# Optimization experiments

Measured on AMD Instinct MI355X. Metric: run time of the kernel, lower is better.

The kernel has to match this reference:

```python
import jax, jax.numpy as jnp
import numpy as np

H = 2048      # hidden_size
NH = 32       # num attention heads
KVH = 8       # num kv heads
HD = 64       # head_dim
G = NH // KVH # kv groups (4)
EPS = 1e-6
THETA = 1000000.0


def _rms_norm(x, g):
    # normalize over last dim (head_dim)
    var = jnp.mean(jnp.square(x), axis=-1, keepdims=True)
    return x * jax.lax.rsqrt(var + EPS) * g


def _rope(seq_len, dtype):
    inv_freq = 1.0 / (THETA ** (jnp.arange(0, HD, 2, dtype=jnp.float32) / HD))
    pos = jnp.arange(seq_len, dtype=jnp.float32)
    freqs = pos[:, None] * inv_freq[None, :]          # [S, HD/2]
    emb = jnp.concatenate([freqs, freqs], axis=-1)    # [S, HD]
    return jnp.cos(emb).astype(dtype), jnp.sin(emb).astype(dtype)


def _rotate_half(x):
    x1, x2 = jnp.split(x, 2, axis=-1)
    return jnp.concatenate([-x2, x1], axis=-1)


def setup_inputs() -> dict:
    key = jax.random.key(0)
    ks = jax.random.split(key, 8)
    B, S = 1, 2048
    s = lambda fan_in: 1.0 / np.sqrt(fan_in)
    return {
        "hidden_states": jax.random.normal(ks[0], (B, S, H), jnp.float32),
        "Wq": jax.random.normal(ks[1], (H, NH * HD + NH), jnp.float32) * s(H),
        "Wk": jax.random.normal(ks[2], (H, KVH * HD), jnp.float32) * s(H),
        "Wv": jax.random.normal(ks[3], (H, KVH * HD), jnp.float32) * s(H),
        "Wo": jax.random.normal(ks[4], (NH * HD, H), jnp.float32) * s(NH * HD),
        "g_q": jnp.ones((HD,), jnp.float32),
        "g_k": jnp.ones((HD,), jnp.float32),
    }


def reference(hidden_states, Wq, Wk, Wv, Wo, g_q, g_k):
    B, S, _ = hidden_states.shape
    dtype = hidden_states.dtype

    qg = hidden_states @ Wq                              # [B,S,NH*HD+NH]
    k = hidden_states @ Wk                               # [B,S,KVH*HD]
    v = hidden_states @ Wv

    # headwise gate split, grouped per kv head (matches torch view/split)
    qg = qg.reshape(B, S, KVH, G * HD + G)
    q, gate = qg[..., : G * HD], qg[..., G * HD :]       # gate: [B,S,KVH,G]
    gate = gate.reshape(B, S, NH, 1)
    q = q.reshape(B, S, NH, HD).transpose(0, 2, 1, 3)    # [B,NH,S,HD]
    k = k.reshape(B, S, KVH, HD).transpose(0, 2, 1, 3)   # [B,KVH,S,HD]
    v = v.reshape(B, S, KVH, HD).transpose(0, 2, 1, 3)

    q = _rms_norm(q, g_q)
    k = _rms_norm(k, g_k)

    cos, sin = _rope(S, dtype)                           # [S,HD]
    cos, sin = cos[None, None], sin[None, None]
    q = q * cos + _rotate_half(q) * sin
    k = k * cos + _rotate_half(k) * sin

    # GQA: repeat kv heads
    k = jnp.repeat(k, G, axis=1)                         # [B,NH,S,HD]
    v = jnp.repeat(v, G, axis=1)

    # causal SDPA
    scale = 1.0 / np.sqrt(HD)
    scores = jnp.einsum("bhqd,bhkd->bhqk", q, k) * scale
    causal = jnp.tril(jnp.ones((S, S), bool))
    scores = jnp.where(causal[None, None], scores, jnp.finfo(dtype).min)
    probs = jax.nn.softmax(scores, axis=-1)
    attn = jnp.einsum("bhqk,bhkd->bhqd", probs, v)       # [B,NH,S,HD]

    attn = attn.transpose(0, 2, 1, 3)                    # [B,S,NH,HD]
    attn = attn * jax.nn.sigmoid(gate)
    attn = attn.reshape(B, S, NH * HD)
    return attn @ Wo
```

## Files before the change

### kernel.cpp

```cpp
#include <hip/hip_runtime.h>
#include <hip/hip_bf16.h>

#define SLEN 2048
#define HDIM 2048
#define NHEAD 32
#define KVHEAD 8
#define HEADD 64
#define NTOT 3104
#define NPAD 3200

typedef short bh8 __attribute__((ext_vector_type(8)));
typedef float f32x4 __attribute__((ext_vector_type(4)));

#define QSCALE 0.1803368801111204f

__device__ __forceinline__ unsigned short f2bf(float f) {
    union { float f; unsigned int u; } v; v.f = f;
    unsigned int u = v.u;
    return (unsigned short)((u + 0x7fffu + ((u >> 16) & 1u)) >> 16);
}

__device__ __forceinline__ unsigned int cvtpk_bf16(float lo, float hi) {
    unsigned int r;
    asm("v_cvt_pk_bf16_f32 %0, %1, %2" : "=v"(r) : "v"(lo), "v"(hi));
    return r;
}

__device__ __forceinline__ void gl_lds16(const unsigned short* g, unsigned short* l) {
    __builtin_amdgcn_global_load_lds(
        (const __attribute__((address_space(1))) unsigned int*)g,
        (__attribute__((address_space(3))) unsigned int*)l, 16, 0, 0);
}

__global__ void rope_tab_k(float* __restrict__ tab) {
    int i = blockIdx.x * 256 + threadIdx.x;
    int s = i >> 5, d = i & 31;
    float invf = __expf(-(float)d * (0.03125f * 13.815510557964274f));
    float ang = (float)s * invf;
    tab[(size_t)i * 2] = cosf(ang);
    tab[(size_t)i * 2 + 1] = sinf(ang);
}

__global__ void cast_x_k(const float* __restrict__ src, unsigned short* __restrict__ dst, int n) {
    int i = blockIdx.x * blockDim.x + threadIdx.x;
    int base = i * 4;
    if (base < n) {
        float4 f = *(const float4*)(src + base);
        ushort4 o;
        o.x = f2bf(f.x); o.y = f2bf(f.y); o.z = f2bf(f.z); o.w = f2bf(f.w);
        *(ushort4*)(dst + base) = o;
    }
}

__global__ void pack_wt_k(const float* __restrict__ Wq, const float* __restrict__ Wk,
                          const float* __restrict__ Wv, unsigned short* __restrict__ Wt) {
    __shared__ float tile[32][33];
    int n0 = blockIdx.x * 32, k0 = blockIdx.y * 32;
    int t = threadIdx.x;
    for (int i = 0; i < 4; i++) {
        int idx = i * 256 + t;
        int kr = idx >> 5, nc = idx & 31;
        int n = n0 + nc, k = k0 + kr;
        float val = 0.f;
        if (n < 2048)       { int h = n >> 6, d = n & 63; val = Wq[(size_t)k * 2080 + (h >> 2) * 260 + (h & 3) * 64 + d]; }
        else if (n < 2560)  { val = Wk[(size_t)k * 512 + (n - 2048)]; }
        else if (n < 3072)  { val = Wv[(size_t)k * 512 + (n - 2560)]; }
        else if (n < 3104)  { int h = n - 3072;           val = Wq[(size_t)k * 2080 + (h >> 2) * 260 + 256 + (h & 3)]; }
        tile[kr][nc] = val;
    }
    __syncthreads();
    for (int i = 0; i < 4; i++) {
        int idx = i * 256 + t;
        int nr = idx >> 5, kc = idx & 31;
        Wt[(size_t)(n0 + nr) * HDIM + (k0 + kc)] = f2bf(tile[kc][nr]);
    }
}

__global__ void pack_wot_k(const float* __restrict__ Wo, unsigned short* __restrict__ Wt) {
    __shared__ float tile[32][33];
    int n0 = blockIdx.x * 32, k0 = blockIdx.y * 32;
    int t = threadIdx.x;
    for (int i = 0; i < 4; i++) {
        int idx = i * 256 + t;
        int kr = idx >> 5, nc = idx & 31;
        tile[kr][nc] = Wo[(size_t)(k0 + kr) * 2048 + (n0 + nc)];
    }
    __syncthreads();
    for (int i = 0; i < 4; i++) {
        int idx = i * 256 + t;
        int nr = idx >> 5, kc = idx & 31;
        Wt[(size_t)(n0 + nr) * 2048 + (k0 + kc)] = f2bf(tile[kc][nr]);
    }
}

template<int NST, bool FUSE>
__global__ __launch_bounds__(256) void gemm_nt64_k(const unsigned short* __restrict__ A,
                                                   const unsigned short* __restrict__ Bt,
                                                   float* __restrict__ C0,
                                                   float* __restrict__ C1,
                                                   int ldc, int mtiles, int ntiles,
                                                   unsigned short* __restrict__ Qr,
                                                   unsigned short* __restrict__ Kr,
                                                   float* __restrict__ gate,
                                                   const float* __restrict__ g_q,
                                                   const float* __restrict__ g_k,
                                                   const float* __restrict__ tab) {
    const int K = 2048;
    __shared__ unsigned short As[3][64 * 32];
    __shared__ unsigned short Bs[3][128 * 32];
    int d = blockIdx.x;
    int nwg = gridDim.x;
    int cpx = nwg >> 3;
    int swz = (d & 7) * cpx + (d >> 3);
    int half = (swz >= ntiles) ? 1 : 0;
    int tile = swz - half * ntiles;
    int m0 = (tile % mtiles) * 64, n0 = (tile / mtiles) * 128;
    float* C = half ? C1 : C0;
    int koff = half * (NST * 32);
    int t = threadIdx.x;
    int w = t >> 6, l = t & 63;
    int wm = (w >> 1) * 32, wn = (w & 1) * 64;
    int lrow = l & 15, lc = l >> 4;
    int rsw = (lrow >> 1) & 3;
    int scol = ((l & 3) ^ ((l >> 3) & 3)) * 8;

    f32x4 acc[2][4];
    #pragma unroll
    for (int i = 0; i < 2; i++)
        #pragma unroll
        for (int j = 0; j < 4; j++)
            acc[i][j] = {0.f, 0.f, 0.f, 0.f};

    const unsigned short* ga = &A[(size_t)(m0 + w * 16 + (l >> 2)) * K + koff + scol];
    const unsigned short* gb = &Bt[(size_t)(n0 + w * 32 + (l >> 2)) * K + koff + scol];

#define STAGE_NT64(s, b) do { \
        gl_lds16(ga + (size_t)(s) * 32,                  &As[b][w * 512]); \
        gl_lds16(gb + (size_t)(s) * 32,                  &Bs[b][(w * 2 + 0) * 512]); \
        gl_lds16(gb + (size_t)(s) * 32 + 16 * (size_t)K, &Bs[b][(w * 2 + 1) * 512]); \
    } while (0)

#define GBODY(rb) do { \
        bh8 af[2], bb[4]; \
        _Pragma("unroll") \
        for (int i = 0; i < 2; i++) \
            af[i] = *(const bh8*)(&As[rb][(wm + i * 16 + lrow) * 32 + ((lc ^ rsw) * 8)]); \
        _Pragma("unroll") \
        for (int j = 0; j < 4; j++) \
            bb[j] = *(const bh8*)(&Bs[rb][(wn + j * 16 + lrow) * 32 + ((lc ^ rsw) * 8)]); \
        _Pragma("unroll") \
        for (int i = 0; i < 2; i++) \
            _Pragma("unroll") \
            for (int j = 0; j < 4; j++) \
                acc[i][j] = __builtin_amdgcn_mfma_f32_16x16x32_bf16(af[i], bb[j], acc[i][j], 0, 0, 0); \
    } while (0)

#define WB3 asm volatile("s_waitcnt vmcnt(3)\n\ts_barrier" ::: "memory")

    STAGE_NT64(0, 0);
    STAGE_NT64(1, 1);
    if constexpr (NST == 64) {
        for (int sb = 0; sb < 60; sb += 3) {
            WB3;
            STAGE_NT64(sb + 2, 2);
            GBODY(0);
            WB3;
            STAGE_NT64(sb + 3, 0);
            GBODY(1);
            WB3;
            STAGE_NT64(sb + 4, 1);
            GBODY(2);
        }
        WB3;
        STAGE_NT64(62, 2);
        GBODY(0);
        WB3;
        STAGE_NT64(63, 0);
        GBODY(1);
        WB3;
        GBODY(2);
        asm volatile("s_waitcnt vmcnt(0)\n\ts_barrier" ::: "memory");
        GBODY(0);
    } else {
        for (int sb = 0; sb < 30; sb += 3) {
            WB3;
            STAGE_NT64(sb + 2, 2);
            GBODY(0);
            WB3;
            STAGE_NT64(sb + 3, 0);
            GBODY(1);
            WB3;
            STAGE_NT64(sb + 4, 1);
            GBODY(2);
        }
        WB3;
        GBODY(0);
        asm volatile("s_waitcnt vmcnt(0)\n\ts_barrier" ::: "memory");
        GBODY(1);
    }
#undef WB3
#undef STAGE_NT64
#undef GBODY
    int col = l & 15, rbase = (l >> 4) * 4;
    if constexpr (FUSE) {
        int nt = n0 >> 7;
        if (nt < 20) {
            bool isQ = nt < 16;
            int hd = ((n0 + wn) - (isQ ? 0 : 2048)) >> 6;
            unsigned short* dst = (isQ ? Qr : Kr) + (size_t)hd * SLEN * 64;
            const float* gv = isQ ? g_q : g_k;
            float g0 = gv[col], g1 = gv[col + 16], g2 = gv[col + 32], g3 = gv[col + 48];
            float qs = isQ ? QSCALE : 1.0f;
            #pragma unroll
            for (int i = 0; i < 2; i++)
                #pragma unroll
                for (int r = 0; r < 4; r++) {
                    int s = m0 + wm + i * 16 + rbase + r;
                    float x0 = acc[i][0][r], x1 = acc[i][1][r];
                    float x2 = acc[i][2][r], x3 = acc[i][3][r];
                    float sq = x0 * x0 + x1 * x1 + x2 * x2 + x3 * x3;
                    sq += __shfl_xor(sq, 1);
                    sq += __shfl_xor(sq, 2);
                    sq += __shfl_xor(sq, 4);
                    sq += __shfl_xor(sq, 8);
                    float inv = rsqrtf(sq * (1.f / 64.f) + 1e-6f);
                    float xn0 = x0 * inv * g0, xn1 = x1 * inv * g1;
                    float xn2 = x2 * inv * g2, xn3 = x3 * inv * g3;
                    const float* te = tab + (size_t)s * 64;
                    float2 cs0 = *(const float2*)(te + col * 2);
                    float2 cs1 = *(const float2*)(te + (col + 16) * 2);
                    unsigned short* dr = dst + (size_t)s * 64;
                    dr[col]      = f2bf((xn0 * cs0.x - xn2 * cs0.y) * qs);
                    dr[col + 16] = f2bf((xn1 * cs1.x - xn3 * cs1.y) * qs);
                    dr[col + 32] = f2bf((xn2 * cs0.x + xn0 * cs0.y) * qs);
                    dr[col + 48] = f2bf((xn3 * cs1.x + xn1 * cs1.y) * qs);
                }
        } else if (nt < 24) {
            for (int i = 0; i < 2; i++)
                for (int j = 0; j < 4; j++)
                    #pragma unroll
                    for (int r = 0; r < 4; r++)
                        C[(size_t)(m0 + wm + i * 16 + rbase + r) * ldc + (n0 + wn + j * 16 + col)] = acc[i][j][r];
        } else {
            if (wn == 0) {
                #pragma unroll
                for (int i = 0; i < 2; i++)
                    #pragma unroll
                    for (int j = 0; j < 2; j++)
                        #pragma unroll
                        for (int r = 0; r < 4; r++) {
                            int s = m0 + wm + i * 16 + rbase + r;
                            int h = j * 16 + col;
                            gate[s * 32 + h] = 1.f / (1.f + __expf(-acc[i][j][r]));
                        }
            }
        }
    } else {
        for (int i = 0; i < 2; i++)
            for (int j = 0; j < 4; j++)
                #pragma unroll
                for (int r = 0; r < 4; r++)
                    C[(size_t)(m0 + wm + i * 16 + rbase + r) * ldc + (n0 + wn + j * 16 + col)] = acc[i][j][r];
    }
}

__global__ void addf4_k(const float* __restrict__ a, const float* __restrict__ b,
                        float* __restrict__ o) {
    int i = (blockIdx.x * 256 + threadIdx.x) * 4;
    float4 x = *(const float4*)(a + i);
    float4 y = *(const float4*)(b + i);
    float4 r; r.x = x.x + y.x; r.y = x.y + y.y; r.z = x.z + y.z; r.w = x.w + y.w;
    *(float4*)(o + i) = r;
}

__global__ void vt_k(const float* __restrict__ QKVG, unsigned short* __restrict__ Vt) {
    __shared__ float tile[64][65];
    int s0 = blockIdx.x * 64, hh = blockIdx.y;
    int t = threadIdx.x;
    #pragma unroll
    for (int i = 0; i < 4; i++) {
        int idx = i * 256 + t;
        int sr = idx >> 4, c4 = (idx & 15) * 4;
        float4 f = *(const float4*)(&QKVG[(size_t)(s0 + sr) * NPAD + 2560 + hh * 64 + c4]);
        tile[sr][c4] = f.x; tile[sr][c4 + 1] = f.y; tile[sr][c4 + 2] = f.z; tile[sr][c4 + 3] = f.w;
    }
    __syncthreads();
    #pragma unroll
    for (int i = 0; i < 4; i++) {
        int idx = i * 256 + t;
        int dr = idx >> 4, c4 = (idx & 15) * 4;
        int hb = c4 >> 5, f = (c4 >> 4) & 1, g = (c4 >> 2) & 3;
        int p = (hb * 4 + g) * 8 + f * 4;
        ushort4 o;
        o.x = f2bf(tile[c4][dr]); o.y = f2bf(tile[c4 + 1][dr]);
        o.z = f2bf(tile[c4 + 2][dr]); o.w = f2bf(tile[c4 + 3][dr]);
        *(ushort4*)(&Vt[((size_t)hh * 64 + dr) * SLEN + s0 + p]) = o;
    }
}

__global__ __launch_bounds__(256) void attn_k(const unsigned short* __restrict__ Qr,
                                              const unsigned short* __restrict__ Kr,
                                              const unsigned short* __restrict__ Vt,
                                              const float* __restrict__ gate,
                                              unsigned short* __restrict__ attn) {
    __shared__ unsigned short Kls[3][64 * 64];
    __shared__ unsigned short Vls[3][64 * 64];
    int d = blockIdx.x;
    int kvh = d & 7;
    int h = kvh * 4 + ((d >> 3) & 3);
    int qt = 31 - (d >> 5);
    int t = threadIdx.x, w = t >> 6, l = t & 63;
    int ql = l & 15, g = l >> 4;
    const float NEGINF = -__builtin_inff();

    const unsigned short* Kh = Kr + (size_t)kvh * SLEN * 64;
    const unsigned short* Vh = Vt + (size_t)kvh * 64 * SLEN;
    const unsigned short* Qh = Qr + (size_t)h * SLEN * 64;
    int lk = g * 8;
    int r8 = l >> 3, c8 = l & 7;
    int cs = 8 * (c8 ^ r8);
    int R0 = w * 16, R1 = w * 16 + 8;
    int rdswz = (ql & 7) << 4;

    int q0 = qt * 64;
    int qrow = q0 + w * 16 + ql;

    bh8 qa0 = *(const bh8*)(Qh + (size_t)qrow * 64 + lk);
    bh8 qa1 = *(const bh8*)(Qh + (size_t)qrow * 64 + 32 + lk);

    f32x4 o[4];
    #pragma unroll
    for (int i = 0; i < 4; i++) o[i] = {0.f, 0.f, 0.f, 0.f};
    float m2 = NEGINF, lsum = 0.f;

    int ntiles = qt + 1;
    {
        gl_lds16(&Kh[(size_t)(0 + R0 + r8) * 64 + cs], &Kls[0][R0 * 64]);
        gl_lds16(&Kh[(size_t)(0 + R1 + r8) * 64 + cs], &Kls[0][R1 * 64]);
        gl_lds16(&Vh[(size_t)(R0 + r8) * SLEN + 0 + cs], &Vls[0][R0 * 64]);
        gl_lds16(&Vh[(size_t)(R1 + r8) * SLEN + 0 + cs], &Vls[0][R1 * 64]);
    }
    if (ntiles > 1) {
        gl_lds16(&Kh[(size_t)(64 + R0 + r8) * 64 + cs], &Kls[1][R0 * 64]);
        gl_lds16(&Kh[(size_t)(64 + R1 + r8) * 64 + cs], &Kls[1][R1 * 64]);
        gl_lds16(&Vh[(size_t)(R0 + r8) * SLEN + 64 + cs], &Vls[1][R0 * 64]);
        gl_lds16(&Vh[(size_t)(R1 + r8) * SLEN + 64 + cs], &Vls[1][R1 * 64]);
    }
    int rd = 0, wr = 2;

    for (int ti = 0; ti < ntiles; ti++) {
        if (ti + 1 < ntiles) asm volatile("s_waitcnt vmcnt(4)\n\ts_barrier" ::: "memory");
        else                 asm volatile("s_waitcnt vmcnt(0)\n\ts_barrier" ::: "memory");
        if (ti + 2 < ntiles) {
            int kv1 = (ti + 2) * 64;
            gl_lds16(&Kh[(size_t)(kv1 + R0 + r8) * 64 + cs], &Kls[wr][R0 * 64]);
            gl_lds16(&Kh[(size_t)(kv1 + R1 + r8) * 64 + cs], &Kls[wr][R1 * 64]);
            gl_lds16(&Vh[(size_t)(R0 + r8) * SLEN + kv1 + cs], &Vls[wr][R0 * 64]);
            gl_lds16(&Vh[(size_t)(R1 + r8) * SLEN + kv1 + cs], &Vls[wr][R1 * 64]);
        }
        const unsigned short* Kb = &Kls[rd][0];
        const unsigned short* Vb = &Vls[rd][0];
        int kv0 = ti * 64;
        f32x4 sct[4];
        __builtin_amdgcn_s_setprio(1);
        #pragma unroll
        for (int nt = 0; nt < 4; nt++) {
            int rb = (nt * 16 + ql) * 128;
            bh8 kb0 = *(const bh8*)(&Kb[(rb + ((g * 16) ^ rdswz)) >> 1]);
            bh8 kb1 = *(const bh8*)(&Kb[(rb + ((64 + g * 16) ^ rdswz)) >> 1]);
            f32x4 a = {0.f, 0.f, 0.f, 0.f};
            a = __builtin_amdgcn_mfma_f32_16x16x32_bf16(kb0, qa0, a, 0, 0, 0);
            a = __builtin_amdgcn_mfma_f32_16x16x32_bf16(kb1, qa1, a, 0, 0, 0);
            sct[nt] = a;
        }
        __builtin_amdgcn_s_setprio(0);
        if (ti == qt) {
            #pragma unroll
            for (int nt = 0; nt < 4; nt++)
                #pragma unroll
                for (int j = 0; j < 4; j++) {
                    int key = kv0 + nt * 16 + 4 * g + j;
                    if (key > qrow) sct[nt][j] = NEGINF;
                }
        }
        float mt0 = fmaxf(fmaxf(sct[0][0], sct[0][1]), fmaxf(sct[0][2], sct[0][3]));
        float mt1 = fmaxf(fmaxf(sct[1][0], sct[1][1]), fmaxf(sct[1][2], sct[1][3]));
        float mt2 = fmaxf(fmaxf(sct[2][0], sct[2][1]), fmaxf(sct[2][2], sct[2][3]));
        float mt3 = fmaxf(fmaxf(sct[3][0], sct[3][1]), fmaxf(sct[3][2], sct[3][3]));
        float mt = fmaxf(fmaxf(mt0, mt1), fmaxf(mt2, mt3));
        mt = fmaxf(mt, __shfl_xor(mt, 16));
        mt = fmaxf(mt, __shfl_xor(mt, 32));
        if (!__all(mt - m2 <= 8.f)) {
            float mnew = fmaxf(m2, mt);
            float resc = __builtin_amdgcn_exp2f(m2 - mnew);
            m2 = mnew;
            lsum *= resc;
            float rf[4];
            #pragma unroll
            for (int j = 0; j < 4; j++) rf[j] = __shfl(resc, 4 * g + j);
            #pragma unroll
            for (int nt = 0; nt < 4; nt++) {
                f32x4 oo = o[nt];
                #pragma unroll
                for (int j = 0; j < 4; j++) oo[j] *= rf[j];
                o[nt] = oo;
            }
        }
        float ps = 0.f;
        #pragma unroll
        for (int nt = 0; nt < 4; nt++)
            #pragma unroll
            for (int j = 0; j < 4; j++) {
                float p = __builtin_amdgcn_exp2f(sct[nt][j] - m2);
                sct[nt][j] = p;
                ps += p;
            }
        ps += __shfl_xor(ps, 16);
        ps += __shfl_xor(ps, 32);
        lsum += ps;
        union { unsigned int u[4]; bh8 v; } pa0, pa1;
        pa0.u[0] = cvtpk_bf16(sct[0][0], sct[0][1]);
        pa0.u[1] = cvtpk_bf16(sct[0][2], sct[0][3]);
        pa0.u[2] = cvtpk_bf16(sct[1][0], sct[1][1]);
        pa0.u[3] = cvtpk_bf16(sct[1][2], sct[1][3]);
        pa1.u[0] = cvtpk_bf16(sct[2][0], sct[2][1]);
        pa1.u[1] = cvtpk_bf16(sct[2][2], sct[2][3]);
        pa1.u[2] = cvtpk_bf16(sct[3][0], sct[3][1]);
        pa1.u[3] = cvtpk_bf16(sct[3][2], sct[3][3]);
        __builtin_amdgcn_s_setprio(1);
        #pragma unroll
        for (int nt = 0; nt < 4; nt++) {
            int rb = (nt * 16 + ql) * 128;
            bh8 vb0 = *(const bh8*)(&Vb[(rb + ((g * 16) ^ rdswz)) >> 1]);
            bh8 vb1 = *(const bh8*)(&Vb[(rb + ((64 + g * 16) ^ rdswz)) >> 1]);
            o[nt] = __builtin_amdgcn_mfma_f32_16x16x32_bf16(pa0.v, vb0, o[nt], 0, 0, 0);
            o[nt] = __builtin_amdgcn_mfma_f32_16x16x32_bf16(pa1.v, vb1, o[nt], 0, 0, 0);
        }
        __builtin_amdgcn_s_setprio(0);
        rd = (rd == 2) ? 0 : rd + 1;
        wr = (wr == 2) ? 0 : wr + 1;
    }

    float gf[4];
    #pragma unroll
    for (int j = 0; j < 4; j++) {
        float ls = __shfl(lsum, 4 * g + j);
        int row = q0 + w * 16 + 4 * g + j;
        gf[j] = gate[row * 32 + h] / ls;
    }
    #pragma unroll
    for (int j = 0; j < 4; j++) {
        int row = q0 + w * 16 + 4 * g + j;
        #pragma unroll
        for (int nt = 0; nt < 4; nt++)
            attn[(size_t)row * 2048 + h * 64 + nt * 16 + ql] = f2bf(o[nt][j] * gf[j]);
    }
}

extern "C" void kernel_launch(void* const* d_in, const int* in_sizes, int n_in,
                              void* d_out, int out_size, void* d_ws, size_t ws_size,
                              hipStream_t stream) {
    const float* hidden = (const float*)d_in[0];
    const float* Wq = (const float*)d_in[1];
    const float* Wk = (const float*)d_in[2];
    const float* Wv = (const float*)d_in[3];
    const float* Wo = (const float*)d_in[4];
    const float* gq = (const float*)d_in[5];
    const float* gk = (const float*)d_in[6];
    float* out = (float*)d_out;
    char* ws = (char*)d_ws;

    unsigned short* X     = (unsigned short*)(ws + 0);
    unsigned short* Wt    = (unsigned short*)(ws + 8388608);
    float*          QKVG  = (float*)(ws + 21495808);
    unsigned short* Qr    = (unsigned short*)(ws + 47710208);
    unsigned short* Kr    = (unsigned short*)(ws + 56098816);
    unsigned short* Vt    = (unsigned short*)(ws + 58195968);
    float*          gate  = (float*)(ws + 60293120);
    unsigned short* attnb = (unsigned short*)(ws + 60555264);
    unsigned short* Wot   = (unsigned short*)(ws + 68943872);
    float*          P1    = (float*)(ws + 77332480);
    float*          rtab  = (float*)(ws + 94109696);
    float*          P0    = QKVG;

    rope_tab_k<<<dim3(256), dim3(256), 0, stream>>>(rtab);
    cast_x_k<<<dim3(4096), dim3(256), 0, stream>>>(hidden, X, SLEN * HDIM);
    pack_wt_k<<<dim3(100, 64), dim3(256), 0, stream>>>(Wq, Wk, Wv, Wt);
    pack_wot_k<<<dim3(64, 64), dim3(256), 0, stream>>>(Wo, Wot);
    gemm_nt64_k<64, true><<<dim3(800), dim3(256), 0, stream>>>(X, Wt, QKVG, QKVG, NPAD, 32, 800,
                                                               Qr, Kr, gate, gq, gk, rtab);
    vt_k<<<dim3(32, 8), dim3(256), 0, stream>>>(QKVG, Vt);
    attn_k<<<dim3(1024), dim3(256), 0, stream>>>(Qr, Kr, Vt, gate, attnb);
    gemm_nt64_k<32, false><<<dim3(1024), dim3(256), 0, stream>>>(attnb, Wot, P0, P1, 2048, 32, 512,
                                                                 nullptr, nullptr, nullptr, nullptr, nullptr, nullptr);
    addf4_k<<<dim3(4096), dim3(256), 0, stream>>>(P0, P1, out);
}
```

Before: 160.9 us.

## Process two adjacent query tiles per attention block to reuse K/V loads

Each attention workgroup now handles two consecutive 64-row query tiles (2u and 2u+1) instead of one. Every K/V tile staged in LDS is used for both tiles' QK and PV MFMAs, and the final diagonal tile is processed for the second query tile alone. This halves the grid and removes about half of the K/V global-to-LDS traffic and barriers. In exchange it doubles accumulator register pressure, which may reduce occupancy, and the smaller grid gives less parallelism and coarser load balance.

```diff
diff --git a/kernel.cpp b/kernel.cpp
--- a/kernel.cpp
+++ b/kernel.cpp
@@ -308,7 +308,9 @@
     int d = blockIdx.x;
     int kvh = d & 7;
     int h = kvh * 4 + ((d >> 3) & 3);
-    int qt = 31 - (d >> 5);
+    int u = 15 - (d >> 5);
+    int qta = 2 * u, qtb = 2 * u + 1;
+    int T = qtb + 1;
     int t = threadIdx.x, w = t >> 6, l = t & 63;
     int ql = l & 15, g = l >> 4;
     const float NEGINF = -__builtin_inff();
@@ -322,36 +324,34 @@
     int R0 = w * 16, R1 = w * 16 + 8;
     int rdswz = (ql & 7) << 4;
 
-    int q0 = qt * 64;
-    int qrow = q0 + w * 16 + ql;
-
-    bh8 qa0 = *(const bh8*)(Qh + (size_t)qrow * 64 + lk);
-    bh8 qa1 = *(const bh8*)(Qh + (size_t)qrow * 64 + 32 + lk);
-
-    f32x4 o[4];
+    int q0a = qta * 64, q0b = qtb * 64;
+    int qrowa = q0a + w * 16 + ql;
+    int qrowb = q0b + w * 16 + ql;
+
+    bh8 qaA0 = *(const bh8*)(Qh + (size_t)qrowa * 64 + lk);
+    bh8 qaA1 = *(const bh8*)(Qh + (size_t)qrowa * 64 + 32 + lk);
+    bh8 qaB0 = *(const bh8*)(Qh + (size_t)qrowb * 64 + lk);
+    bh8 qaB1 = *(const bh8*)(Qh + (size_t)qrowb * 64 + 32 + lk);
+
+    f32x4 oA[4], oB[4];
     #pragma unroll
-    for (int i = 0; i < 4; i++) o[i] = {0.f, 0.f, 0.f, 0.f};
-    float m2 = NEGINF, lsum = 0.f;
-
-    int ntiles = qt + 1;
-    {
-        gl_lds16(&Kh[(size_t)(0 + R0 + r8) * 64 + cs], &Kls[0][R0 * 64]);
-        gl_lds16(&Kh[(size_t)(0 + R1 + r8) * 64 + cs], &Kls[0][R1 * 64]);
-        gl_lds16(&Vh[(size_t)(R0 + r8) * SLEN + 0 + cs], &Vls[0][R0 * 64]);
-        gl_lds16(&Vh[(size_t)(R1 + r8) * SLEN + 0 + cs], &Vls[0][R1 * 64]);
-    }
-    if (ntiles > 1) {
-        gl_lds16(&Kh[(size_t)(64 + R0 + r8) * 64 + cs], &Kls[1][R0 * 64]);
-        gl_lds16(&Kh[(size_t)(64 + R1 + r8) * 64 + cs], &Kls[1][R1 * 64]);
-        gl_lds16(&Vh[(size_t)(R0 + r8) * SLEN + 64 + cs], &Vls[1][R0 * 64]);
-        gl_lds16(&Vh[(size_t)(R1 + r8) * SLEN + 64 + cs], &Vls[1][R1 * 64]);
-    }
+    for (int i = 0; i < 4; i++) { oA[i] = {0.f, 0.f, 0.f, 0.f}; oB[i] = {0.f, 0.f, 0.f, 0.f}; }
+    float m2a = NEGINF, lsa = 0.f;
+    float m2b = NEGINF, lsb = 0.f;
+
+    gl_lds16(&Kh[(size_t)(0 + R0 + r8) * 64 + cs], &Kls[0][R0 * 64]);
+    gl_lds16(&Kh[(size_t)(0 + R1 + r8) * 64 + cs], &Kls[0][R1 * 64]);
+    gl_lds16(&Vh[(size_t)(R0 + r8) * SLEN + 0 + cs], &Vls[0][R0 * 64]);
+    gl_lds16(&Vh[(size_t)(R1 + r8) * SLEN + 0 + cs], &Vls[0][R1 * 64]);
+    gl_lds16(&Kh[(size_t)(64 + R0 + r8) * 64 + cs], &Kls[1][R0 * 64]);
+    gl_lds16(&Kh[(size_t)(64 + R1 + r8) * 64 + cs], &Kls[1][R1 * 64]);
+    gl_lds16(&Vh[(size_t)(R0 + r8) * SLEN + 64 + cs], &Vls[1][R0 * 64]);
+    gl_lds16(&Vh[(size_t)(R1 + r8) * SLEN + 64 + cs], &Vls[1][R1 * 64]);
     int rd = 0, wr = 2;
 
-    for (int ti = 0; ti < ntiles; ti++) {
-        if (ti + 1 < ntiles) asm volatile("s_waitcnt vmcnt(4)\n\ts_barrier" ::: "memory");
-        else                 asm volatile("s_waitcnt vmcnt(0)\n\ts_barrier" ::: "memory");
-        if (ti + 2 < ntiles) {
+    for (int ti = 0; ti < T - 1; ti++) {
+        asm volatile("s_waitcnt vmcnt(4)\n\ts_barrier" ::: "memory");
+        if (ti + 2 < T) {
             int kv1 = (ti + 2) * 64;
             gl_lds16(&Kh[(size_t)(kv1 + R0 + r8) * 64 + cs], &Kls[wr][R0 * 64]);
             gl_lds16(&Kh[(size_t)(kv1 + R1 + r8) * 64 + cs], &Kls[wr][R1 * 64]);
@@ -361,7 +361,7 @@
         const unsigned short* Kb = &Kls[rd][0];
         const unsigned short* Vb = &Vls[rd][0];
         int kv0 = ti * 64;
-        f32x4 sct[4];
+        f32x4 sa[4], sb[4];
         __builtin_amdgcn_s_setprio(1);
         #pragma unroll
         for (int nt = 0; nt < 4; nt++) {
@@ -369,41 +369,169 @@
             bh8 kb0 = *(const bh8*)(&Kb[(rb + ((g * 16) ^ rdswz)) >> 1]);
             bh8 kb1 = *(const bh8*)(&Kb[(rb + ((64 + g * 16) ^ rdswz)) >> 1]);
             f32x4 a = {0.f, 0.f, 0.f, 0.f};
-            a = __builtin_amdgcn_mfma_f32_16x16x32_bf16(kb0, qa0, a, 0, 0, 0);
-            a = __builtin_amdgcn_mfma_f32_16x16x32_bf16(kb1, qa1, a, 0, 0, 0);
-            sct[nt] = a;
+            a = __builtin_amdgcn_mfma_f32_16x16x32_bf16(kb0, qaA0, a, 0, 0, 0);
+            a = __builtin_amdgcn_mfma_f32_16x16x32_bf16(kb1, qaA1, a, 0, 0, 0);
+            sa[nt] = a;
+            f32x4 b = {0.f, 0.f, 0.f, 0.f};
+            b = __builtin_amdgcn_mfma_f32_16x16x32_bf16(kb0, qaB0, b, 0, 0, 0);
+            b = __builtin_amdgcn_mfma_f32_16x16x32_bf16(kb1, qaB1, b, 0, 0, 0);
+            sb[nt] = b;
         }
         __builtin_amdgcn_s_setprio(0);
-        if (ti == qt) {
+        if (ti == qta) {
             #pragma unroll
             for (int nt = 0; nt < 4; nt++)
                 #pragma unroll
                 for (int j = 0; j < 4; j++) {
                     int key = kv0 + nt * 16 + 4 * g + j;
-                    if (key > qrow) sct[nt][j] = NEGINF;
+                    if (key > qrowa) sa[nt][j] = NEGINF;
                 }
         }
-        float mt0 = fmaxf(fmaxf(sct[0][0], sct[0][1]), fmaxf(sct[0][2], sct[0][3]));
-        float mt1 = fmaxf(fmaxf(sct[1][0], sct[1][1]), fmaxf(sct[1][2], sct[1][3]));
-        float mt2 = fmaxf(fmaxf(sct[2][0], sct[2][1]), fmaxf(sct[2][2], sct[2][3]));
-        float mt3 = fmaxf(fmaxf(sct[3][0], sct[3][1]), fmaxf(sct[3][2], sct[3][3]));
+        {
+            float mt0 = fmaxf(fmaxf(sa[0][0], sa[0][1]), fmaxf(sa[0][2], sa[0][3]));
+            float mt1 = fmaxf(fmaxf(sa[1][0], sa[1][1]), fmaxf(sa[1][2], sa[1][3]));
+            float mt2 = fmaxf(fmaxf(sa[2][0], sa[2][1]), fmaxf(sa[2][2], sa[2][3]));
+            float mt3 = fmaxf(fmaxf(sa[3][0], sa[3][1]), fmaxf(sa[3][2], sa[3][3]));
+            float mt = fmaxf(fmaxf(mt0, mt1), fmaxf(mt2, mt3));
+            mt = fmaxf(mt, __shfl_xor(mt, 16));
+            mt = fmaxf(mt, __shfl_xor(mt, 32));
+            if (!__all(mt - m2a <= 8.f)) {
+                float mnew = fmaxf(m2a, mt);
+                float resc = __builtin_amdgcn_exp2f(m2a - mnew);
+                m2a = mnew;
+                lsa *= resc;
+                float rf[4];
+                #pragma unroll
+                for (int j = 0; j < 4; j++) rf[j] = __shfl(resc, 4 * g + j);
+                #pragma unroll
+                for (int nt = 0; nt < 4; nt++) {
+                    f32x4 oo = oA[nt];
+                    #pragma unroll
+                    for (int j = 0; j < 4; j++) oo[j] *= rf[j];
+                    oA[nt] = oo;
+                }
+            }
+            float ps = 0.f;
+            #pragma unroll
+            for (int nt = 0; nt < 4; nt++)
+                #pragma unroll
+                for (int j = 0; j < 4; j++) {
+                    float p = __builtin_amdgcn_exp2f(sa[nt][j] - m2a);
+                    sa[nt][j] = p;
+                    ps += p;
+                }
+            ps += __shfl_xor(ps, 16);
+            ps += __shfl_xor(ps, 32);
+            lsa += ps;
+        }
+        {
+            float mt0 = fmaxf(fmaxf(sb[0][0], sb[0][1]), fmaxf(sb[0][2], sb[0][3]));
+            float mt1 = fmaxf(fmaxf(sb[1][0], sb[1][1]), fmaxf(sb[1][2], sb[1][3]));
+            float mt2 = fmaxf(fmaxf(sb[2][0], sb[2][1]), fmaxf(sb[2][2], sb[2][3]));
+            float mt3 = fmaxf(fmaxf(sb[3][0], sb[3][1]), fmaxf(sb[3][2], sb[3][3]));
+            float mt = fmaxf(fmaxf(mt0, mt1), fmaxf(mt2, mt3));
+            mt = fmaxf(mt, __shfl_xor(mt, 16));
+            mt = fmaxf(mt, __shfl_xor(mt, 32));
+            if (!__all(mt - m2b <= 8.f)) {
+                float mnew = fmaxf(m2b, mt);
+                float resc = __builtin_amdgcn_exp2f(m2b - mnew);
+                m2b = mnew;
+                lsb *= resc;
+                float rf[4];
+                #pragma unroll
+                for (int j = 0; j < 4; j++) rf[j] = __shfl(resc, 4 * g + j);
+                #pragma unroll
+                for (int nt = 0; nt < 4; nt++) {
+                    f32x4 oo = oB[nt];
+                    #pragma unroll
+                    for (int j = 0; j < 4; j++) oo[j] *= rf[j];
+                    oB[nt] = oo;
+                }
+            }
+            float ps = 0.f;
+            #pragma unroll
+            for (int nt = 0; nt < 4; nt++)
+                #pragma unroll
+                for (int j = 0; j < 4; j++) {
+                    float p = __builtin_amdgcn_exp2f(sb[nt][j] - m2b);
+                    sb[nt][j] = p;
+                    ps += p;
+                }
+            ps += __shfl_xor(ps, 16);
+            ps += __shfl_xor(ps, 32);
+            lsb += ps;
+        }
+        union { unsigned int uu[4]; bh8 v; } pa0, pa1, pb0, pb1;
+        pa0.uu[0] = cvtpk_bf16(sa[0][0], sa[0][1]); pa0.uu[1] = cvtpk_bf16(sa[0][2], sa[0][3]);
+        pa0.uu[2] = cvtpk_bf16(sa[1][0], sa[1][1]); pa0.uu[3] = cvtpk_bf16(sa[1][2], sa[1][3]);
+        pa1.uu[0] = cvtpk_bf16(sa[2][0], sa[2][1]); pa1.uu[1] = cvtpk_bf16(sa[2][2], sa[2][3]);
+        pa1.uu[2] = cvtpk_bf16(sa[3][0], sa[3][1]); pa1.uu[3] = cvtpk_bf16(sa[3][2], sa[3][3]);
+        pb0.uu[0] = cvtpk_bf16(sb[0][0], sb[0][1]); pb0.uu[1] = cvtpk_bf16(sb[0][2], sb[0][3]);
+        pb0.uu[2] = cvtpk_bf16(sb[1][0], sb[1][1]); pb0.uu[3] = cvtpk_bf16(sb[1][2], sb[1][3]);
+        pb1.uu[0] = cvtpk_bf16(sb[2][0], sb[2][1]); pb1.uu[1] = cvtpk_bf16(sb[2][2], sb[2][3]);
+        pb1.uu[2] = cvtpk_bf16(sb[3][0], sb[3][1]); pb1.uu[3] = cvtpk_bf16(sb[3][2], sb[3][3]);
+        __builtin_amdgcn_s_setprio(1);
+        #pragma unroll
+        for (int nt = 0; nt < 4; nt++) {
+            int rb = (nt * 16 + ql) * 128;
+            bh8 vb0 = *(const bh8*)(&Vb[(rb + ((g * 16) ^ rdswz)) >> 1]);
+            bh8 vb1 = *(const bh8*)(&Vb[(rb + ((64 + g * 16) ^ rdswz)) >> 1]);
+            oA[nt] = __builtin_amdgcn_mfma_f32_16x16x32_bf16(pa0.v, vb0, oA[nt], 0, 0, 0);
+            oA[nt] = __builtin_amdgcn_mfma_f32_16x16x32_bf16(pa1.v, vb1, oA[nt], 0, 0, 0);
+            oB[nt] = __builtin_amdgcn_mfma_f32_16x16x32_bf16(pb0.v, vb0, oB[nt], 0, 0, 0);
+            oB[nt] = __builtin_amdgcn_mfma_f32_16x16x32_bf16(pb1.v, vb1, oB[nt], 0, 0, 0);
+        }
+        __builtin_amdgcn_s_setprio(0);
+        rd = (rd == 2) ? 0 : rd + 1;
+        wr = (wr == 2) ? 0 : wr + 1;
+    }
+
+    {
+        asm volatile("s_waitcnt vmcnt(0)\n\ts_barrier" ::: "memory");
+        const unsigned short* Kb = &Kls[rd][0];
+        const unsigned short* Vb = &Vls[rd][0];
+        int kv0 = qtb * 64;
+        f32x4 sb[4];
+        __builtin_amdgcn_s_setprio(1);
+        #pragma unroll
+        for (int nt = 0; nt < 4; nt++) {
+            int rb = (nt * 16 + ql) * 128;
+            bh8 kb0 = *(const bh8*)(&Kb[(rb + ((g * 16) ^ rdswz)) >> 1]);
+            bh8 kb1 = *(const bh8*)(&Kb[(rb + ((64 + g * 16) ^ rdswz)) >> 1]);
+            f32x4 b = {0.f, 0.f, 0.f, 0.f};
+            b = __builtin_amdgcn_mfma_f32_16x16x32_bf16(kb0, qaB0, b, 0, 0, 0);
+            b = __builtin_amdgcn_mfma_f32_16x16x32_bf16(kb1, qaB1, b, 0, 0, 0);
+            sb[nt] = b;
+        }
+        __builtin_amdgcn_s_setprio(0);
+        #pragma unroll
+        for (int nt = 0; nt < 4; nt++)
+            #pragma unroll
+            for (int j = 0; j < 4; j++) {
+                int key = kv0 + nt * 16 + 4 * g + j;
+                if (key > qrowb) sb[nt][j] = NEGINF;
+            }
+        float mt0 = fmaxf(fmaxf(sb[0][0], sb[0][1]), fmaxf(sb[0][2], sb[0][3]));
+        float mt1 = fmaxf(fmaxf(sb[1][0], sb[1][1]), fmaxf(sb[1][2], sb[1][3]));
+        float mt2 = fmaxf(fmaxf(sb[2][0], sb[2][1]), fmaxf(sb[2][2], sb[2][3]));
+        float mt3 = fmaxf(fmaxf(sb[3][0], sb[3][1]), fmaxf(sb[3][2], sb[3][3]));
         float mt = fmaxf(fmaxf(mt0, mt1), fmaxf(mt2, mt3));
         mt = fmaxf(mt, __shfl_xor(mt, 16));
         mt = fmaxf(mt, __shfl_xor(mt, 32));
-        if (!__all(mt - m2 <= 8.f)) {
-            float mnew = fmaxf(m2, mt);
-            float resc = __builtin_amdgcn_exp2f(m2 - mnew);
-            m2 = mnew;
-            lsum *= resc;
+        if (!__all(mt - m2b <= 8.f)) {
+            float mnew = fmaxf(m2b, mt);
+            float resc = __builtin_amdgcn_exp2f(m2b - mnew);
+            m2b = mnew;
+            lsb *= resc;
             float rf[4];
             #pragma unroll
             for (int j = 0; j < 4; j++) rf[j] = __shfl(resc, 4 * g + j);
             #pragma unroll
             for (int nt = 0; nt < 4; nt++) {
-                f32x4 oo = o[nt];
+                f32x4 oo = oB[nt];
                 #pragma unroll
                 for (int j = 0; j < 4; j++) oo[j] *= rf[j];
-                o[nt] = oo;
+                oB[nt] = oo;
             }
         }
         float ps = 0.f;
@@ -411,49 +539,61 @@
         for (int nt = 0; nt < 4; nt++)
             #pragma unroll
             for (int j = 0; j < 4; j++) {
-                float p = __builtin_amdgcn_exp2f(sct[nt][j] - m2);
-                sct[nt][j] = p;
+                float p = __builtin_amdgcn_exp2f(sb[nt][j] - m2b);
+                sb[nt][j] = p;
                 ps += p;
             }
         ps += __shfl_xor(ps, 16);
         ps += __shfl_xor(ps, 32);
-        lsum += ps;
-        union { unsigned int u[4]; bh8 v; } pa0, pa1;
-        pa0.u[0] = cvtpk_bf16(sct[0][0], sct[0][1]);
-        pa0.u[1] = cvtpk_bf16(sct[0][2], sct[0][3]);
-        pa0.u[2] = cvtpk_bf16(sct[1][0], sct[1][1]);
-        pa0.u[3] = cvtpk_bf16(sct[1][2], sct[1][3]);
-        pa1.u[0] = cvtpk_bf16(sct[2][0], sct[2][1]);
-        pa1.u[1] = cvtpk_bf16(sct[2][2], sct[2][3]);
-        pa1.u[2] = cvtpk_bf16(sct[3][0], sct[3][1]);
-        pa1.u[3] = cvtpk_bf16(sct[3][2], sct[3][3]);
+        lsb += ps;
+        union { unsigned int uu[4]; bh8 v; } pb0, pb1;
+        pb0.uu[0] = cvtpk_bf16(sb[0][0], sb[0][1]); pb0.uu[1] = cvtpk_bf16(sb[0][2], sb[0][3]);
+        pb0.uu[2] = cvtpk_bf16(sb[1][0], sb[1][1]); pb0.uu[3] = cvtpk_bf16(sb[1][2], sb[1][3]);
+        pb1.uu[0] = cvtpk_bf16(sb[2][0], sb[2][1]); pb1.uu[1] = cvtpk_bf16(sb[2][2], sb[2][3]);
+        pb1.uu[2] = cvtpk_bf16(sb[3][0], sb[3][1]); pb1.uu[3] = cvtpk_bf16(sb[3][2], sb[3][3]);
         __builtin_amdgcn_s_setprio(1);
         #pragma unroll
         for (int nt = 0; nt < 4; nt++) {
             int rb = (nt * 16 + ql) * 128;
             bh8 vb0 = *(const bh8*)(&Vb[(rb + ((g * 16) ^ rdswz)) >> 1]);
             bh8 vb1 = *(const bh8*)(&Vb[(rb + ((64 + g * 16) ^ rdswz)) >> 1]);
-            o[nt] = __builtin_amdgcn_mfma_f32_16x16x32_bf16(pa0.v, vb0, o[nt], 0, 0, 0);
-            o[nt] = __builtin_amdgcn_mfma_f32_16x16x32_bf16(pa1.v, vb1, o[nt], 0, 0, 0);
+            oB[nt] = __builtin_amdgcn_mfma_f32_16x16x32_bf16(pb0.v, vb0, oB[nt], 0, 0, 0);
+            oB[nt] = __builtin_amdgcn_mfma_f32_16x16x32_bf16(pb1.v, vb1, oB[nt], 0, 0, 0);
         }
         __builtin_amdgcn_s_setprio(0);
-        rd = (rd == 2) ? 0 : rd + 1;
-        wr = (wr == 2) ? 0 : wr + 1;
-    }
-
-    float gf[4];
-    #pragma unroll
-    for (int j = 0; j < 4; j++) {
-        float ls = __shfl(lsum, 4 * g + j);
-        int row = q0 + w * 16 + 4 * g + j;
-        gf[j] = gate[row * 32 + h] / ls;
-    }
-    #pragma unroll
-    for (int j = 0; j < 4; j++) {
-        int row = q0 + w * 16 + 4 * g + j;
-        #pragma unroll
-        for (int nt = 0; nt < 4; nt++)
-            attn[(size_t)row * 2048 + h * 64 + nt * 16 + ql] = f2bf(o[nt][j] * gf[j]);
+    }
+
+    {
+        float gf[4];
+        #pragma unroll
+        for (int j = 0; j < 4; j++) {
+            float ls = __shfl(lsa, 4 * g + j);
+            int row = q0a + w * 16 + 4 * g + j;
+            gf[j] = gate[row * 32 + h] / ls;
+        }
+        #pragma unroll
+        for (int j = 0; j < 4; j++) {
+            int row = q0a + w * 16 + 4 * g + j;
+            #pragma unroll
+            for (int nt = 0; nt < 4; nt++)
+                attn[(size_t)row * 2048 + h * 64 + nt * 16 + ql] = f2bf(oA[nt][j] * gf[j]);
+        }
+    }
+    {
+        float gf[4];
+        #pragma unroll
+        for (int j = 0; j < 4; j++) {
+            float ls = __shfl(lsb, 4 * g + j);
+            int row = q0b + w * 16 + 4 * g + j;
+            gf[j] = gate[row * 32 + h] / ls;
+        }
+        #pragma unroll
+        for (int j = 0; j < 4; j++) {
+            int row = q0b + w * 16 + 4 * g + j;
+            #pragma unroll
+            for (int nt = 0; nt < 4; nt++)
+                attn[(size_t)row * 2048 + h * 64 + nt * 16 + ql] = f2bf(oB[nt][j] * gf[j]);
+        }
     }
 }
 
@@ -490,7 +630,7 @@
     gemm_nt64_k<64, true><<<dim3(800), dim3(256), 0, stream>>>(X, Wt, QKVG, QKVG, NPAD, 32, 800,
                                                                Qr, Kr, gate, gq, gk, rtab);
     vt_k<<<dim3(32, 8), dim3(256), 0, stream>>>(QKVG, Vt);
-    attn_k<<<dim3(1024), dim3(256), 0, stream>>>(Qr, Kr, Vt, gate, attnb);
+    attn_k<<<dim3(512), dim3(256), 0, stream>>>(Qr, Kr, Vt, gate, attnb);
     gemm_nt64_k<32, false><<<dim3(1024), dim3(256), 0, stream>>>(attnb, Wot, P0, P1, 2048, 32, 512,
                                                                  nullptr, nullptr, nullptr, nullptr, nullptr, nullptr);
     addf4_k<<<dim3(4096), dim3(256), 0, stream>>>(P0, P1, out);
```

New measurement: 171.8 us. 6.8% more time.
